# Kernel optimization log

Hardware: AMD Instinct MI355X
Metric: run time of the kernel (lower is better)

Reference implementation:

```python
import jax, jax.numpy as jnp
import numpy as np

N = 100000       # nodes
E = 1600000      # edges (avg degree 16)
F_IN = 128       # num_node_features
H = 128          # hidden_num
C = 40           # num_classes


def setup_inputs() -> dict:
    key = jax.random.key(0)
    k = jax.random.split(key, 6)
    x = jax.random.normal(k[0], (N, F_IN), dtype=jnp.float32)
    edge_index = jax.random.randint(k[1], (2, E), 0, N, dtype=jnp.int32)
    # Glorot-ish scaled params for the two GCNConv layers
    W1 = jax.random.normal(k[2], (F_IN, H), dtype=jnp.float32) * (1.0 / np.sqrt(F_IN))
    b1 = jnp.zeros((H,), dtype=jnp.float32)
    W2 = jax.random.normal(k[3], (H, C), dtype=jnp.float32) * (1.0 / np.sqrt(H))
    b2 = jnp.zeros((C,), dtype=jnp.float32)
    return {"x": x, "edge_index": edge_index, "W1": W1, "b1": b1, "W2": W2, "b2": b2}


def _gcn_conv(x, W, b, src, dst, n_nodes):
    """PyG GCNConv: add self-loops, symmetric normalization, linear transform.
    out[i] = sum_{j in N(i)} d_i^-1/2 d_j^-1/2 (x W)[j] + d_i^-1 (x W)[i] + b
    Self-loop contribution handled analytically (no edge concat).
    """
    h = x @ W                                            # [N, out]
    ones = jnp.ones((src.shape[0],), dtype=x.dtype)
    deg = jax.ops.segment_sum(ones, dst, num_segments=n_nodes) + 1.0  # +1 self-loop
    dinv = jax.lax.rsqrt(deg)                            # deg >= 1 always
    norm = dinv[src] * dinv[dst]                         # [E]
    msg = h[src] * norm[:, None]                         # [E, out] gather + scale
    agg = jax.ops.segment_sum(msg, dst, num_segments=n_nodes)
    agg = agg + h * (dinv * dinv)[:, None]               # self-loop term
    return agg + b


def reference(x, edge_index, W1, b1, W2, b2):
    # eval mode: F.dropout(training=False) is identity
    src, dst = edge_index[0], edge_index[1]
    h = jax.nn.relu(_gcn_conv(x, W1, b1, src, dst, N))
    out = _gcn_conv(h, W2, b2, src, dst, N)
    return out
```

## Files before the change

kernel.cpp:

```cpp
#include <hip/hip_runtime.h>
#include <hip/hip_fp16.h>


#define F_IN  128
#define F_H   128
#define F_OUT 40

#define BK_SHIFT 7
#define BK_MAX   1024

typedef _Float16 half8v __attribute__((ext_vector_type(8)));
typedef float    f32x4  __attribute__((ext_vector_type(4)));


__global__ void k_prep(const float* __restrict__ W1, const float* __restrict__ W2,
                       __half* __restrict__ img1, __half* __restrict__ img2,
                       int* __restrict__ bcnt, int nbk) {
    int b = blockIdx.x;
    if (b < 64) {
        int idx = b * 256 + threadIdx.x;
        int j = idx >> 7, k = idx & 127;
        img1[j * 128 + (k ^ ((j & 7) << 3))] = __float2half_rn(W1[k * 128 + j]);
    } else if (b < 88) {
        int idx = (b - 64) * 256 + threadIdx.x;
        int j = idx >> 7, k = idx & 127;
        float v = (j < F_OUT) ? W2[k * F_OUT + j] : 0.f;
        img2[j * 128 + (k ^ ((j & 7) << 3))] = __float2half_rn(v);
    } else {
        for (int i = threadIdx.x; i < nbk; i += 256) bcnt[i] = 0;
    }
}


#define CHUNK 4096

__global__ __launch_bounds__(256) void k_bscatter(const int* __restrict__ src,
                                                  const int* __restrict__ dst,
                                                  int* __restrict__ bcnt,
                                                  int* __restrict__ ebuf,
                                                  int e, int nbk, int cap) {
    __shared__ int hist[BK_MAX];
    __shared__ int base[BK_MAX];
    __shared__ int run[BK_MAX];
    int e0 = blockIdx.x * CHUNK;
    int e1 = min(e0 + CHUNK, e);
    for (int i = threadIdx.x; i < nbk; i += 256) { hist[i] = 0; run[i] = 0; }
    __syncthreads();
    for (int i = e0 + threadIdx.x; i < e1; i += 256)
        atomicAdd(&hist[dst[i] >> BK_SHIFT], 1);
    __syncthreads();
    for (int i = threadIdx.x; i < nbk; i += 256) {
        int c = hist[i];
        base[i] = c ? (cap * i + atomicAdd(&bcnt[i], c)) : 0;
    }
    __syncthreads();
    for (int i = e0 + threadIdx.x; i < e1; i += 256) {
        int d = dst[i];
        int b = d >> BK_SHIFT;
        int r = atomicAdd(&run[b], 1);
        ebuf[base[b] + r] = (src[i] << BK_SHIFT) | (d & ((1 << BK_SHIFT) - 1));
    }
}


__global__ __launch_bounds__(256) void k_bnode(const int* __restrict__ ebuf,
                                               const int* __restrict__ bcnt,
                                               int2* __restrict__ rbd,
                                               float* __restrict__ dinv,
                                               int* __restrict__ col,
                                               int n, int cap) {
    __shared__ int hist[128];
    __shared__ int sc[128];
    __shared__ int cur[128];
    const int b   = blockIdx.x;
    const int tid = threadIdx.x;
    const int e0 = b * cap;
    const int e1 = e0 + bcnt[b];

    if (tid < 128) hist[tid] = 0;
    __syncthreads();
    for (int i = e0 + tid; i < e1; i += 256)
        atomicAdd(&hist[ebuf[i] & 127], 1);
    __syncthreads();
    if (tid < 128) sc[tid] = hist[tid];
    __syncthreads();
    for (int off = 1; off < 128; off <<= 1) {
        int t = 0;
        if (tid < 128 && tid >= off) t = sc[tid - off];
        __syncthreads();
        if (tid < 128) sc[tid] += t;
        __syncthreads();
    }
    if (tid < 128) {
        int node = (b << BK_SHIFT) + tid;
        int excl = sc[tid] - hist[tid];
        if (node < n) {
            rbd[node] = make_int2(e0 + excl, hist[tid]);
            dinv[node] = rsqrtf((float)hist[tid] + 1.0f);
        }
        cur[tid] = e0 + excl;
    }
    __syncthreads();
    for (int i = e0 + tid; i < e1; i += 256) {
        int w = ebuf[i];
        int pos = atomicAdd(&cur[w & 127], 1);
        col[pos] = w >> BK_SHIFT;
    }
}


__global__ __launch_bounds__(256) void k_gemm1(const float* __restrict__ x,
                                               const __half* __restrict__ Wimg,
                                               const float* __restrict__ dinv,
                                               __half* __restrict__ h, int n) {
    __shared__ __half wlds[128 * 128];
    const int tid = threadIdx.x;
#pragma unroll
    for (int it = 0; it < 8; ++it) {
        int i = tid * 8 + it * 2048;
        *(uint4*)&wlds[i] = *(const uint4*)&Wimg[i];
    }

    const int l  = tid & 63;
    const int g  = l >> 4;
    const int r0 = blockIdx.x * 64 + (tid >> 6) * 16;
    int row = r0 + (l & 15);
    if (row > n - 1) row = n - 1;

    const float* xb = x + row * F_IN + g * 8;
    half8v afr[4];
#pragma unroll
    for (int kk = 0; kk < 4; ++kk) {
        float4 u0 = *(const float4*)(xb + kk * 32);
        float4 u1 = *(const float4*)(xb + kk * 32 + 4);
        half8v a;
        a[0] = (_Float16)u0.x; a[1] = (_Float16)u0.y;
        a[2] = (_Float16)u0.z; a[3] = (_Float16)u0.w;
        a[4] = (_Float16)u1.x; a[5] = (_Float16)u1.y;
        a[6] = (_Float16)u1.z; a[7] = (_Float16)u1.w;
        afr[kk] = a;
    }
    __syncthreads();

    const char* wb = (const char*)wlds;
    const int swz = (l & 7) << 4;
    f32x4 acc[8] = {};
#pragma unroll
    for (int ct = 0; ct < 8; ++ct) {
        const int base = (ct * 16 + (l & 15)) * 256;
#pragma unroll
        for (int kk = 0; kk < 4; ++kk) {
            half8v bfr = *(const half8v*)(wb + base + ((kk * 64 + g * 16) ^ swz));
            acc[ct] = __builtin_amdgcn_mfma_f32_16x16x32_f16(afr[kk], bfr, acc[ct], 0, 0, 0);
        }
    }

    const int orow0 = r0 + g * 4;
    float dv[4];
#pragma unroll
    for (int b = 0; b < 4; ++b) {
        int r = orow0 + b;
        dv[b] = (r < n) ? dinv[r] : 0.f;
    }
#pragma unroll
    for (int ct = 0; ct < 8; ++ct) {
#pragma unroll
        for (int b = 0; b < 4; ++b) {
            int r = orow0 + b;
            if (r < n)
                h[r * F_H + ct * 16 + (l & 15)] = __float2half_rn(acc[ct][b] * dv[b]);
        }
    }
}


__global__ __launch_bounds__(256) void k_agg1(const __half* __restrict__ h1s,
                                              const int2* __restrict__ rbd,
                                              const float* __restrict__ dinv,
                                              const float* __restrict__ b1,
                                              __half* __restrict__ out1, int n) {
    int wid = (blockIdx.x * 256 + threadIdx.x) >> 6;
    int lane = threadIdx.x & 63;
    if (wid >= n) return;
    int2 bd = rbd[wid];
    int beg = bd.x, end = bd.x + bd.y;
    const __half2* hb = (const __half2*)h1s + lane;
    const int* colp = 0;
    (void)colp;

    extern __shared__ char _dummy[];
    const int* col = (const int*)nullptr;
    (void)col;

    float a0x = 0.f, a0y = 0.f, a1x = 0.f, a1y = 0.f;
    float a2x = 0.f, a2y = 0.f, a3x = 0.f, a3y = 0.f;
    (void)a0x;
}

__global__ __launch_bounds__(256) void k_agg1r(const __half* __restrict__ h1s,
                                               const int2* __restrict__ rbd,
                                               const int* __restrict__ col,
                                               const float* __restrict__ dinv,
                                               const float* __restrict__ b1,
                                               __half* __restrict__ out1, int n) {
    int wid = (blockIdx.x * 256 + threadIdx.x) >> 6;
    int lane = threadIdx.x & 63;
    if (wid >= n) return;
    int2 bd = rbd[wid];
    int beg = bd.x, end = bd.x + bd.y;
    const __half2* hb = (const __half2*)h1s + lane;

    float a0x = 0.f, a0y = 0.f, a1x = 0.f, a1y = 0.f;
    float a2x = 0.f, a2y = 0.f, a3x = 0.f, a3y = 0.f;
    int idx = beg;
    for (; idx + 12 <= end; idx += 12) {
        int s[12];
#pragma unroll
        for (int j = 0; j < 12; ++j) s[j] = col[idx + j];
        float2 v[12];
#pragma unroll
        for (int j = 0; j < 12; ++j) v[j] = __half22float2(hb[s[j] << 6]);
#pragma unroll
        for (int j = 0; j < 12; ++j) {
            if ((j & 3) == 0) { a0x += v[j].x; a0y += v[j].y; }
            else if ((j & 3) == 1) { a1x += v[j].x; a1y += v[j].y; }
            else if ((j & 3) == 2) { a2x += v[j].x; a2y += v[j].y; }
            else { a3x += v[j].x; a3y += v[j].y; }
        }
    }
    if (idx + 6 <= end) {
        int s[6];
#pragma unroll
        for (int j = 0; j < 6; ++j) s[j] = col[idx + j];
        float2 v[6];
#pragma unroll
        for (int j = 0; j < 6; ++j) v[j] = __half22float2(hb[s[j] << 6]);
        a0x += v[0].x; a0y += v[0].y; a1x += v[1].x; a1y += v[1].y;
        a2x += v[2].x; a2y += v[2].y; a3x += v[3].x; a3y += v[3].y;
        a0x += v[4].x; a0y += v[4].y; a1x += v[5].x; a1y += v[5].y;
        idx += 6;
    }
    for (; idx < end; ++idx) {
        float2 v = __half22float2(hb[col[idx] << 6]);
        a0x += v.x; a0y += v.y;
    }
    float2 hv = __half22float2(hb[wid << 6]);
    float ax = (((a0x + a1x) + (a2x + a3x)) + hv.x);
    float ay = (((a0y + a1y) + (a2y + a3y)) + hv.y);
    float di = dinv[wid];
    int c2 = lane * 2;
    ax = fmaf(ax, di, b1[c2]);
    ay = fmaf(ay, di, b1[c2 + 1]);
    __half2 o = __floats2half2_rn(fmaxf(ax, 0.f), fmaxf(ay, 0.f));
    *(__half2*)&out1[(wid << 7) + c2] = o;
}


__global__ __launch_bounds__(256) void k_gemm2(const __half* __restrict__ xin,
                                               const __half* __restrict__ Wimg,
                                               const float* __restrict__ dinv,
                                               __half* __restrict__ h, int n) {
    __shared__ __half wlds[48 * 128];
    const int tid = threadIdx.x;
#pragma unroll
    for (int it = 0; it < 3; ++it) {
        int i = tid * 8 + it * 2048;
        *(uint4*)&wlds[i] = *(const uint4*)&Wimg[i];
    }

    const int l  = tid & 63;
    const int g  = l >> 4;
    const int r0 = blockIdx.x * 64 + (tid >> 6) * 16;
    int row = r0 + (l & 15);
    if (row > n - 1) row = n - 1;

    const __half* ab = xin + row * F_H + g * 8;
    half8v afr[4];
#pragma unroll
    for (int kk = 0; kk < 4; ++kk) afr[kk] = *(const half8v*)(ab + kk * 32);
    __syncthreads();

    const char* wb = (const char*)wlds;
    const int swz = (l & 7) << 4;
    f32x4 acc[3] = {};
#pragma unroll
    for (int ct = 0; ct < 3; ++ct) {
        const int base = (ct * 16 + (l & 15)) * 256;
#pragma unroll
        for (int kk = 0; kk < 4; ++kk) {
            half8v bfr = *(const half8v*)(wb + base + ((kk * 64 + g * 16) ^ swz));
            acc[ct] = __builtin_amdgcn_mfma_f32_16x16x32_f16(afr[kk], bfr, acc[ct], 0, 0, 0);
        }
    }

    const int orow0 = r0 + g * 4;
    float dv[4];
#pragma unroll
    for (int b = 0; b < 4; ++b) {
        int r = orow0 + b;
        dv[b] = (r < n) ? dinv[r] : 0.f;
    }
#pragma unroll
    for (int ct = 0; ct < 3; ++ct) {
        int c = ct * 16 + (l & 15);
#pragma unroll
        for (int b = 0; b < 4; ++b) {
            int r = orow0 + b;
            if (r < n && c < F_OUT)
                h[r * F_OUT + c] = __float2half_rn(acc[ct][b] * dv[b]);
        }
    }
}


__global__ __launch_bounds__(256) void k_agg2(const __half* __restrict__ h2s,
                                              const int2* __restrict__ rbd,
                                              const int* __restrict__ col,
                                              const float* __restrict__ dinv,
                                              const float* __restrict__ b2,
                                              float* __restrict__ out, int n) {
    int wid = (blockIdx.x * 256 + threadIdx.x) >> 6;
    int lane = threadIdx.x & 63;
    if (wid >= n) return;
    int third = lane / 20;
    bool act = (third < 3);
    int ll = act ? (lane - third * 20) : 0;
    const __half2* hb = (const __half2*)h2s + ll;
    int2 bd = rbd[wid];
    int beg = bd.x, end = bd.x + bd.y;

    float a0x = 0.f, a0y = 0.f, a1x = 0.f, a1y = 0.f;
    float a2x = 0.f, a2y = 0.f, a3x = 0.f, a3y = 0.f;
    int idx = act ? (beg + third) : end;
    for (; idx + 9 < end; idx += 12) {
        int s0 = col[idx], s1 = col[idx + 3], s2 = col[idx + 6], s3 = col[idx + 9];
        float2 v0 = __half22float2(hb[s0 * 20]);
        float2 v1 = __half22float2(hb[s1 * 20]);
        float2 v2 = __half22float2(hb[s2 * 20]);
        float2 v3 = __half22float2(hb[s3 * 20]);
        a0x += v0.x; a0y += v0.y; a1x += v1.x; a1y += v1.y;
        a2x += v2.x; a2y += v2.y; a3x += v3.x; a3y += v3.y;
    }
    for (; idx < end; idx += 3) {
        float2 v = __half22float2(hb[col[idx] * 20]);
        a0x += v.x; a0y += v.y;
    }
    float tx = (a0x + a1x) + (a2x + a3x);
    float ty = (a0y + a1y) + (a2y + a3y);
    tx += __shfl(tx, lane + 20) + __shfl(tx, lane + 40);
    ty += __shfl(ty, lane + 20) + __shfl(ty, lane + 40);
    if (third == 0) {
        float2 hv = __half22float2(hb[wid * 20]);
        float di = dinv[wid];
        int c2 = ll * 2;
        float2 o;
        o.x = fmaf(tx + hv.x, di, b2[c2]);
        o.y = fmaf(ty + hv.y, di, b2[c2 + 1]);
        *(float2*)&out[wid * F_OUT + c2] = o;
    }
}


extern "C" void kernel_launch(void* const* d_in, const int* in_sizes, int n_in,
                              void* d_out, int out_size, void* d_ws, size_t ws_size,
                              hipStream_t stream) {
    const float* x  = (const float*)d_in[0];
    const int*   ei = (const int*)d_in[1];
    const float* W1 = (const float*)d_in[2];
    const float* b1 = (const float*)d_in[3];
    const float* W2 = (const float*)d_in[4];
    const float* b2 = (const float*)d_in[5];
    float* out = (float*)d_out;

    const int N = in_sizes[0] / F_IN;
    const int E = in_sizes[1] / 2;
    const int* src = ei;
    const int* dst = ei + E;
    const int nbk = (N + (1 << BK_SHIFT) - 1) >> BK_SHIFT;
    const int cap = (((2 * E) / nbk) + 63) & ~63;

    char* ws = (char*)d_ws;
    size_t off = 0;
    auto alloc = [&](size_t bytes) -> void* {
        off = (off + 255) & ~(size_t)255;
        void* p = ws + off;
        off += bytes;
        return p;
    };
    float*  dinv    = (float*) alloc((size_t)N * 4);
    int2*   rbd     = (int2*)  alloc((size_t)N * 8);
    int*    bcnt    = (int*)   alloc(BK_MAX * 4);
    __half* W1img   = (__half*)alloc(128 * 128 * 2);
    __half* W2img   = (__half*)alloc(48 * 128 * 2);
    int*    ebuf    = (int*)   alloc((size_t)nbk * cap * 4);
    int*    col     = (int*)   alloc((size_t)nbk * cap * 4);
    __half* h1s     = (__half*)alloc((size_t)N * F_H * 2);
    __half* out1h   = (__half*)alloc((size_t)N * F_H * 2);
    __half* h2s     = h1s;

    const int gC = (E + CHUNK - 1) / CHUNK;

    k_prep    <<<89, 256, 0, stream>>>(W1, W2, W1img, W2img, bcnt, nbk);
    k_bscatter<<<gC, 256, 0, stream>>>(src, dst, bcnt, ebuf, E, nbk, cap);
    k_bnode   <<<nbk, 256, 0, stream>>>(ebuf, bcnt, rbd, dinv, col, N, cap);

    k_gemm1<<<(N + 63) / 64, 256, 0, stream>>>(x, W1img, dinv, h1s, N);
    k_agg1r<<<(N + 3) / 4, 256, 0, stream>>>(h1s, rbd, col, dinv, b1, out1h, N);
    k_gemm2<<<(N + 63) / 64, 256, 0, stream>>>(out1h, W2img, dinv, h2s, N);
    k_agg2 <<<(N + 3) / 4, 256, 0, stream>>>(h2s, rbd, col, dinv, b2, out, N);
}
```

Baseline: 194.0 us.

## Use wide vector gathers with multi-edge lane groups in both aggregation kernels

Both SpMM aggregation kernels now gather neighbour rows with wider per-lane loads: 16-byte uint4 loads in layer 1, where 4 lane groups each take a different edge, and 8-byte uint2 loads in layer 2, where 6 groups of 10 lanes each take a different edge. Partial sums are combined across groups with shuffles, and the epilogue writes vectorized outputs. This cuts the number of load instructions per edge and processes several edges per wave at once, aiming at higher memory-level parallelism in the gather-bound aggregation. In exchange it adds cross-lane shuffle reductions, and in layer 2 four lanes sit idle. The dead k_agg1 stub is removed.

```diff
diff --git a/kernel.cpp b/kernel.cpp
--- a/kernel.cpp
+++ b/kernel.cpp
@@ -8,6 +8,7 @@
 
 #define BK_SHIFT 7
 #define BK_MAX   1024
+#define CHUNK    4096
 
 typedef _Float16 half8v __attribute__((ext_vector_type(8)));
 typedef float    f32x4  __attribute__((ext_vector_type(4)));
@@ -32,8 +33,6 @@
 }
 
 
-#define CHUNK 4096
-
 __global__ __launch_bounds__(256) void k_bscatter(const int* __restrict__ src,
                                                   const int* __restrict__ dst,
                                                   int* __restrict__ bcnt,
@@ -174,28 +173,13 @@
 }
 
 
-__global__ __launch_bounds__(256) void k_agg1(const __half* __restrict__ h1s,
-                                              const int2* __restrict__ rbd,
-                                              const float* __restrict__ dinv,
-                                              const float* __restrict__ b1,
-                                              __half* __restrict__ out1, int n) {
-    int wid = (blockIdx.x * 256 + threadIdx.x) >> 6;
-    int lane = threadIdx.x & 63;
-    if (wid >= n) return;
-    int2 bd = rbd[wid];
-    int beg = bd.x, end = bd.x + bd.y;
-    const __half2* hb = (const __half2*)h1s + lane;
-    const int* colp = 0;
-    (void)colp;
-
-    extern __shared__ char _dummy[];
-    const int* col = (const int*)nullptr;
-    (void)col;
-
-    float a0x = 0.f, a0y = 0.f, a1x = 0.f, a1y = 0.f;
-    float a2x = 0.f, a2y = 0.f, a3x = 0.f, a3y = 0.f;
-    (void)a0x;
-}
+#define UNPK8(A, u) { \
+    float2 t0 = __half22float2(*(__half2*)&(u).x); \
+    float2 t1 = __half22float2(*(__half2*)&(u).y); \
+    float2 t2 = __half22float2(*(__half2*)&(u).z); \
+    float2 t3 = __half22float2(*(__half2*)&(u).w); \
+    A[0] += t0.x; A[1] += t0.y; A[2] += t1.x; A[3] += t1.y; \
+    A[4] += t2.x; A[5] += t2.y; A[6] += t3.x; A[7] += t3.y; }
 
 __global__ __launch_bounds__(256) void k_agg1r(const __half* __restrict__ h1s,
                                                const int2* __restrict__ rbd,
@@ -208,51 +192,64 @@
     if (wid >= n) return;
     int2 bd = rbd[wid];
     int beg = bd.x, end = bd.x + bd.y;
-    const __half2* hb = (const __half2*)h1s + lane;
-
-    float a0x = 0.f, a0y = 0.f, a1x = 0.f, a1y = 0.f;
-    float a2x = 0.f, a2y = 0.f, a3x = 0.f, a3y = 0.f;
+    const int q = lane >> 4;
+    const int f = lane & 15;
+    const uint4* hb = (const uint4*)h1s + f;
+
+    float ax[8] = {}, bx[8] = {};
     int idx = beg;
-    for (; idx + 12 <= end; idx += 12) {
-        int s[12];
-#pragma unroll
-        for (int j = 0; j < 12; ++j) s[j] = col[idx + j];
-        float2 v[12];
-#pragma unroll
-        for (int j = 0; j < 12; ++j) v[j] = __half22float2(hb[s[j] << 6]);
-#pragma unroll
-        for (int j = 0; j < 12; ++j) {
-            if ((j & 3) == 0) { a0x += v[j].x; a0y += v[j].y; }
-            else if ((j & 3) == 1) { a1x += v[j].x; a1y += v[j].y; }
-            else if ((j & 3) == 2) { a2x += v[j].x; a2y += v[j].y; }
-            else { a3x += v[j].x; a3y += v[j].y; }
-        }
-    }
-    if (idx + 6 <= end) {
-        int s[6];
-#pragma unroll
-        for (int j = 0; j < 6; ++j) s[j] = col[idx + j];
-        float2 v[6];
-#pragma unroll
-        for (int j = 0; j < 6; ++j) v[j] = __half22float2(hb[s[j] << 6]);
-        a0x += v[0].x; a0y += v[0].y; a1x += v[1].x; a1y += v[1].y;
-        a2x += v[2].x; a2y += v[2].y; a3x += v[3].x; a3y += v[3].y;
-        a0x += v[4].x; a0y += v[4].y; a1x += v[5].x; a1y += v[5].y;
-        idx += 6;
-    }
-    for (; idx < end; ++idx) {
-        float2 v = __half22float2(hb[col[idx] << 6]);
-        a0x += v.x; a0y += v.y;
-    }
-    float2 hv = __half22float2(hb[wid << 6]);
-    float ax = (((a0x + a1x) + (a2x + a3x)) + hv.x);
-    float ay = (((a0y + a1y) + (a2y + a3y)) + hv.y);
-    float di = dinv[wid];
-    int c2 = lane * 2;
-    ax = fmaf(ax, di, b1[c2]);
-    ay = fmaf(ay, di, b1[c2 + 1]);
-    __half2 o = __floats2half2_rn(fmaxf(ax, 0.f), fmaxf(ay, 0.f));
-    *(__half2*)&out1[(wid << 7) + c2] = o;
+    for (; idx + 8 <= end; idx += 8) {
+        int s0 = col[idx + q];
+        int s1 = col[idx + 4 + q];
+        uint4 u0 = hb[s0 << 4];
+        uint4 u1 = hb[s1 << 4];
+        UNPK8(ax, u0);
+        UNPK8(bx, u1);
+    }
+    if (idx + 4 <= end) {
+        int s = col[idx + q];
+        uint4 u = hb[s << 4];
+        UNPK8(ax, u);
+        idx += 4;
+    }
+    int rem = end - idx;
+    if (q < rem) {
+        int s = col[idx + q];
+        uint4 u = hb[s << 4];
+        UNPK8(bx, u);
+    }
+#pragma unroll
+    for (int j = 0; j < 8; ++j) ax[j] += bx[j];
+#pragma unroll
+    for (int j = 0; j < 8; ++j) {
+        ax[j] += __shfl(ax[j], lane ^ 16);
+        ax[j] += __shfl(ax[j], lane ^ 32);
+    }
+    if (q == 0) {
+        uint4 hu = hb[wid << 4];
+        float hv[8] = {};
+        UNPK8(hv, hu);
+        float di = dinv[wid];
+        float4 bv0 = *(const float4*)&b1[8 * f];
+        float4 bv1 = *(const float4*)&b1[8 * f + 4];
+        float o[8];
+        o[0] = fmaxf(fmaf(ax[0] + hv[0], di, bv0.x), 0.f);
+        o[1] = fmaxf(fmaf(ax[1] + hv[1], di, bv0.y), 0.f);
+        o[2] = fmaxf(fmaf(ax[2] + hv[2], di, bv0.z), 0.f);
+        o[3] = fmaxf(fmaf(ax[3] + hv[3], di, bv0.w), 0.f);
+        o[4] = fmaxf(fmaf(ax[4] + hv[4], di, bv1.x), 0.f);
+        o[5] = fmaxf(fmaf(ax[5] + hv[5], di, bv1.y), 0.f);
+        o[6] = fmaxf(fmaf(ax[6] + hv[6], di, bv1.z), 0.f);
+        o[7] = fmaxf(fmaf(ax[7] + hv[7], di, bv1.w), 0.f);
+        __half2 p0 = __floats2half2_rn(o[0], o[1]);
+        __half2 p1 = __floats2half2_rn(o[2], o[3]);
+        __half2 p2 = __floats2half2_rn(o[4], o[5]);
+        __half2 p3 = __floats2half2_rn(o[6], o[7]);
+        uint4 pk;
+        pk.x = *(unsigned int*)&p0; pk.y = *(unsigned int*)&p1;
+        pk.z = *(unsigned int*)&p2; pk.w = *(unsigned int*)&p3;
+        *(uint4*)&out1[(wid << 7) + 8 * f] = pk;
+    }
 }
 
 
@@ -312,6 +309,11 @@
     }
 }
 
+
+#define UNPK4(A, u) { \
+    float2 t0 = __half22float2(*(__half2*)&(u).x); \
+    float2 t1 = __half22float2(*(__half2*)&(u).y); \
+    A[0] += t0.x; A[1] += t0.y; A[2] += t1.x; A[3] += t1.y; }
 
 __global__ __launch_bounds__(256) void k_agg2(const __half* __restrict__ h2s,
                                               const int2* __restrict__ rbd,
@@ -322,41 +324,56 @@
     int wid = (blockIdx.x * 256 + threadIdx.x) >> 6;
     int lane = threadIdx.x & 63;
     if (wid >= n) return;
-    int third = lane / 20;
-    bool act = (third < 3);
-    int ll = act ? (lane - third * 20) : 0;
-    const __half2* hb = (const __half2*)h2s + ll;
+    int g = lane / 10;
+    int f = lane - g * 10;
+    bool act = (g < 6);
+    const uint2* hb = (const uint2*)h2s + f;
     int2 bd = rbd[wid];
     int beg = bd.x, end = bd.x + bd.y;
 
-    float a0x = 0.f, a0y = 0.f, a1x = 0.f, a1y = 0.f;
-    float a2x = 0.f, a2y = 0.f, a3x = 0.f, a3y = 0.f;
-    int idx = act ? (beg + third) : end;
-    for (; idx + 9 < end; idx += 12) {
-        int s0 = col[idx], s1 = col[idx + 3], s2 = col[idx + 6], s3 = col[idx + 9];
-        float2 v0 = __half22float2(hb[s0 * 20]);
-        float2 v1 = __half22float2(hb[s1 * 20]);
-        float2 v2 = __half22float2(hb[s2 * 20]);
-        float2 v3 = __half22float2(hb[s3 * 20]);
-        a0x += v0.x; a0y += v0.y; a1x += v1.x; a1y += v1.y;
-        a2x += v2.x; a2y += v2.y; a3x += v3.x; a3y += v3.y;
-    }
-    for (; idx < end; idx += 3) {
-        float2 v = __half22float2(hb[col[idx] * 20]);
-        a0x += v.x; a0y += v.y;
-    }
-    float tx = (a0x + a1x) + (a2x + a3x);
-    float ty = (a0y + a1y) + (a2y + a3y);
-    tx += __shfl(tx, lane + 20) + __shfl(tx, lane + 40);
-    ty += __shfl(ty, lane + 20) + __shfl(ty, lane + 40);
-    if (third == 0) {
-        float2 hv = __half22float2(hb[wid * 20]);
+    float ax[4] = {}, bx[4] = {};
+    int idx = beg;
+    if (act) {
+        for (; idx + 12 <= end; idx += 12) {
+            int s0 = col[idx + g];
+            int s1 = col[idx + 6 + g];
+            uint2 u0 = hb[s0 * 10];
+            uint2 u1 = hb[s1 * 10];
+            UNPK4(ax, u0);
+            UNPK4(bx, u1);
+        }
+        if (idx + 6 <= end) {
+            int s = col[idx + g];
+            uint2 u = hb[s * 10];
+            UNPK4(ax, u);
+            idx += 6;
+        }
+        int rem = end - idx;
+        if (g < rem) {
+            int s = col[idx + g];
+            uint2 u = hb[s * 10];
+            UNPK4(bx, u);
+        }
+    }
+#pragma unroll
+    for (int j = 0; j < 4; ++j) ax[j] += bx[j];
+#pragma unroll
+    for (int j = 0; j < 4; ++j) {
+        float t = ax[j] + __shfl(ax[j], lane + 30);
+        ax[j] = t + __shfl(t, lane + 10) + __shfl(t, lane + 20);
+    }
+    if (g == 0) {
+        uint2 hu = hb[wid * 10];
+        float hv[4] = {};
+        UNPK4(hv, hu);
         float di = dinv[wid];
-        int c2 = ll * 2;
-        float2 o;
-        o.x = fmaf(tx + hv.x, di, b2[c2]);
-        o.y = fmaf(ty + hv.y, di, b2[c2 + 1]);
-        *(float2*)&out[wid * F_OUT + c2] = o;
+        float4 bv = *(const float4*)&b2[4 * f];
+        float4 o;
+        o.x = fmaf(ax[0] + hv[0], di, bv.x);
+        o.y = fmaf(ax[1] + hv[1], di, bv.y);
+        o.z = fmaf(ax[2] + hv[2], di, bv.z);
+        o.w = fmaf(ax[3] + hv[3], di, bv.w);
+        *(float4*)&out[wid * F_OUT + 4 * f] = o;
     }
 }
 
```

After: 185.2 us (median of 3 runs). 4.6% less time.
